# Optimization experiments

Hardware: AMD Instinct MI355X
Metric: run time of the kernel (lower is better)

The kernel has to match this reference:

```python
import jax, jax.numpy as jnp
import numpy as np

B, H, S, DK, DV = 2, 16, 2048, 128, 128


def setup_inputs() -> dict:
    key = jax.random.key(0)
    kq, kk, kv = jax.random.split(key, 3)
    query = jax.random.normal(kq, (B, H, S, DK), dtype=jnp.float32)
    k_ = jax.random.normal(kk, (B, H, S, DK), dtype=jnp.float32)
    value = jax.random.normal(kv, (B, H, S, DV), dtype=jnp.float32)
    # causal mask: True = masked out (upper triangle above diagonal)
    causal = ~jnp.tril(jnp.ones((S, S), dtype=bool))
    mask = jnp.broadcast_to(causal[None, None, :, :], (B, 1, S, S))
    return {"query": query, "key": k_, "value": value, "mask": mask}


def reference(query, key, value, mask):
    d_k = query.shape[-1]
    # scores: (B, H, Sq, Sk)
    scores = jnp.einsum("bhqd,bhkd->bhqk", query, key) / jnp.sqrt(jnp.float32(d_k))
    scores = jnp.where(mask, -jnp.inf, scores)
    attention_weights = jax.nn.softmax(scores, axis=-1)
    # dropout p=0.0 (eval) -> identity
    output = jnp.einsum("bhqk,bhkv->bhqv", attention_weights, value)
    return (output, attention_weights)
```

## Files before the change

kernel.cpp:

```cpp
#include <hip/hip_runtime.h>
#include <hip/hip_bf16.h>


typedef __attribute__((ext_vector_type(4))) float  f32x4;
typedef __attribute__((ext_vector_type(8))) short  short8;
typedef __attribute__((ext_vector_type(4))) short  short4v;

#define S_LEN 2048
#define DKK   128
#define QBLK  64
#define KBLK  64
#define NBH   32

__device__ __forceinline__ short f2bf(float f) {
    unsigned u = __builtin_bit_cast(unsigned, f);
    u += 0x7FFF + ((u >> 16) & 1);
    return (short)(u >> 16);
}

__device__ __forceinline__ void g2l16(const void* g, void* l) {
    __builtin_amdgcn_global_load_lds(
        (const __attribute__((address_space(1))) unsigned int*)g,
        (__attribute__((address_space(3))) unsigned int*)l, 16, 0, 0);
}


__global__ __launch_bounds__(256) void conv_k(const float* __restrict__ K,
                                              short* __restrict__ Kb) {
    const int NCH = NBH * S_LEN * (DKK / 8);
    for (int g = blockIdx.x * 256 + threadIdx.x; g < NCH; g += gridDim.x * 256) {
        const int row = g >> 4;
        const int c   = g & 15;
        const float* p = K + (size_t)row * DKK + c * 8;
        f32x4 a = *(const f32x4*)p;
        f32x4 b = *(const f32x4*)(p + 4);
        short8 r;
        #pragma unroll
        for (int j = 0; j < 4; ++j) {
            r[j]     = f2bf(a[j]);
            r[4 + j] = f2bf(b[j]);
        }
        *(short8*)(Kb + (size_t)row * DKK + (size_t)(c ^ (row & 7)) * 8) = r;
    }
}

__global__ __launch_bounds__(256) void conv_vt(const float* __restrict__ V,
                                               short* __restrict__ VT) {
    __shared__ short tile[64][130];
    const int bh = blockIdx.x >> 5;
    const int kt = blockIdx.x & 31;
    const float* Vb = V + ((size_t)bh * S_LEN + kt * 64) * DKK;
    const int t  = threadIdx.x;
    const int k8 = t >> 5, d0 = (t & 31) * 4;
    #pragma unroll
    for (int it = 0; it < 8; ++it) {
        int k = it * 8 + k8;
        f32x4 v = *(const f32x4*)(Vb + (size_t)k * DKK + d0);
        #pragma unroll
        for (int j = 0; j < 4; ++j) tile[k][d0 + j] = f2bf(v[j]);
    }
    __syncthreads();
    const int d = t >> 1, half = t & 1;
    short* outb = VT + (size_t)bh * DKK * S_LEN + (size_t)d * S_LEN + kt * 64;
    #pragma unroll
    for (int cc = 0; cc < 4; ++cc) {
        short8 r;
        #pragma unroll
        for (int j = 0; j < 8; ++j) r[j] = tile[half * 32 + cc * 8 + j][d];
        int cp = (half * 4 + cc) ^ (d & 7);
        *(short8*)(outb + cp * 8) = r;
    }
}


__global__ __launch_bounds__(256) void attn_main(
    const float* __restrict__ Qf, const short* __restrict__ Kb,
    const short* __restrict__ VT, float* __restrict__ O,
    float* __restrict__ W)
{
    __shared__ __align__(16) short kT[2][KBLK * DKK];
    __shared__ __align__(16) short vtT[2][DKK * KBLK];
    __shared__ __align__(16) short pT[4][16 * KBLK];

    const int tid  = threadIdx.x;
    const int lane = tid & 63;
    const int w    = tid >> 6;
    const int lg   = lane >> 4;
    const int lr   = lane & 15;
    const int s7   = lr & 7;

    const int bh = (blockIdx.x & 7) * 4 + ((blockIdx.x >> 3) & 3);
    const int qt = 31 - (blockIdx.x >> 5);
    const int q0 = qt * QBLK;
    const int qbase = q0 + w * 16;
    const int kend  = q0 + QBLK;
    const int ntk   = qt + 1;
    const int qg    = qbase + lr;

    const short* Kbh = Kb + (size_t)bh * S_LEN * DKK;
    const short* VTb = VT + (size_t)bh * DKK * S_LEN;
    float* Ob = O + (size_t)bh * S_LEN * DKK;
    float* Wb = W + (size_t)bh * S_LEN * S_LEN;

    const float QSCALE = 0.08838834764831845f * 1.4426950408889634f;
    short8 qf[4];
    {
        const float* qp = Qf + ((size_t)bh * S_LEN + qg) * DKK + lg * 8;
        #pragma unroll
        for (int ds = 0; ds < 4; ++ds) {
            f32x4 a = *(const f32x4*)(qp + ds * 32);
            f32x4 b = *(const f32x4*)(qp + ds * 32 + 4);
            short8 r;
            #pragma unroll
            for (int jj = 0; jj < 4; ++jj) {
                r[jj]     = f2bf(a[jj] * QSCALE);
                r[4 + jj] = f2bf(b[jj] * QSCALE);
            }
            qf[ds] = r;
        }
    }

    auto stage_k = [&](int buf, int kt_) {
        const char* gk = (const char*)(Kbh + (size_t)kt_ * KBLK * DKK);
        char* lk = (char*)kT[buf];
        #pragma unroll
        for (int i = 0; i < 4; ++i)
            g2l16(gk + i * 4096 + tid * 16, lk + i * 4096 + w * 1024);
    };
    auto stage_v = [&](int buf, int kt_) {
        const char* gv = (const char*)VTb + (size_t)kt_ * (KBLK * 2);
        char* lv = (char*)vtT[buf];
        #pragma unroll
        for (int i = 0; i < 4; ++i) {
            const int L = i * 4096 + tid * 16;
            g2l16(gv + (size_t)(L >> 7) * (S_LEN * 2) + (L & 127),
                  lv + i * 4096 + w * 1024);
        }
    };

    auto k_frag = [&](const char* kBc, int t, int ds) -> short8 {
        const int off = ((16 * t + lr) * 256 + ds * 64 + lg * 16) ^ (s7 << 4);
        return *(const short8*)(kBc + off);
    };

    float lsum = 0.f;
    int cur = 0;
    stage_k(0, 0);
    for (int kt_ = 0; kt_ < ntk; ++kt_) {
        __syncthreads();
        if (kt_ + 1 < ntk) stage_k(cur ^ 1, kt_ + 1);
        const int k0 = kt_ * KBLK;
        const char* kBc = (const char*)kT[cur];
        #pragma unroll
        for (int t = 0; t < 4; ++t) {
            f32x4 d = {0.f, 0.f, 0.f, 0.f};
            __builtin_amdgcn_s_setprio(1);
            #pragma unroll
            for (int ds = 0; ds < 4; ++ds)
                d = __builtin_amdgcn_mfma_f32_16x16x32_bf16(
                        k_frag(kBc, t, ds), qf[ds], d, 0, 0, 0);
            __builtin_amdgcn_s_setprio(0);
            const int kb = k0 + 16 * t + lg * 4;
            #pragma unroll
            for (int r = 0; r < 4; ++r)
                lsum += (kb + r <= qg) ? exp2f(d[r]) : 0.f;
        }
        cur ^= 1;
    }
    lsum += __shfl_xor(lsum, 16);
    lsum += __shfl_xor(lsum, 32);
    const float invl = 1.0f / lsum;

    f32x4 acc[8];
    #pragma unroll
    for (int ii = 0; ii < 8; ++ii) acc[ii] = (f32x4){0.f, 0.f, 0.f, 0.f};

    __syncthreads();
    cur = 0;
    stage_k(0, 0);
    stage_v(0, 0);
    for (int kt_ = 0; kt_ < ntk; ++kt_) {
        __syncthreads();
        if (kt_ + 1 < ntk) { stage_k(cur ^ 1, kt_ + 1); stage_v(cur ^ 1, kt_ + 1); }
        const int k0 = kt_ * KBLK;
        const char* kBc = (const char*)kT[cur];
        const char* vBc = (const char*)vtT[cur];
        char* pBc = (char*)pT[w];

        #pragma unroll
        for (int t = 0; t < 4; ++t) {
            f32x4 d = {0.f, 0.f, 0.f, 0.f};
            __builtin_amdgcn_s_setprio(1);
            #pragma unroll
            for (int ds = 0; ds < 4; ++ds)
                d = __builtin_amdgcn_mfma_f32_16x16x32_bf16(
                        k_frag(kBc, t, ds), qf[ds], d, 0, 0, 0);
            __builtin_amdgcn_s_setprio(0);
            const int kb = k0 + 16 * t + lg * 4;
            f32x4 pv;
            short4v pb;
            #pragma unroll
            for (int r = 0; r < 4; ++r) {
                const float p = (kb + r <= qg) ? exp2f(d[r]) * invl : 0.f;
                pv[r] = p;
                pb[r] = f2bf(p);
            }
            *(f32x4*)(Wb + (size_t)qg * S_LEN + kb) = pv;
            const int poff = lr * 128 + (((16 * t + lg * 4) * 2) ^ (s7 << 4));
            *(short4v*)(pBc + poff) = pb;
        }
        #pragma unroll
        for (int h = 0; h < 2; ++h) {
            const int poff = lr * 128 + ((h * 64 + lg * 16) ^ (s7 << 4));
            short8 pa = *(const short8*)(pBc + poff);
            __builtin_amdgcn_s_setprio(1);
            #pragma unroll
            for (int nt = 0; nt < 8; ++nt) {
                const int voff = (nt * 16 + lr) * 128 + ((h * 64 + lg * 16) ^ (s7 << 4));
                short8 vf = *(const short8*)(vBc + voff);
                acc[nt] = __builtin_amdgcn_mfma_f32_16x16x32_bf16(pa, vf, acc[nt], 0, 0, 0);
            }
            __builtin_amdgcn_s_setprio(0);
        }
        cur ^= 1;
    }

    #pragma unroll
    for (int nt = 0; nt < 8; ++nt)
        #pragma unroll
        for (int r = 0; r < 4; ++r)
            Ob[(size_t)(qbase + lg * 4 + r) * DKK + nt * 16 + lr] = acc[nt][r];

    const int zc = S_LEN - kend;
    if (zc > 0) {
        const int yo = tid >> 2;
        const int xo = tid & 3;
        float* wrow = Wb + (size_t)(q0 + yo) * S_LEN + kend;
        const f32x4 z = {0.f, 0.f, 0.f, 0.f};
        for (int c = xo * 4; c < zc; c += 16)
            *(f32x4*)(wrow + c) = z;
    }
}

extern "C" void kernel_launch(void* const* d_in, const int* in_sizes, int n_in,
                              void* d_out, int out_size, void* d_ws, size_t ws_size,
                              hipStream_t stream) {
    const float* Q = (const float*)d_in[0];
    const float* K = (const float*)d_in[1];
    const float* V = (const float*)d_in[2];
    float* O = (float*)d_out;
    float* W = (float*)d_out + (size_t)NBH * S_LEN * DKK;

    const size_t TEN = (size_t)NBH * S_LEN * DKK;
    short* Kb  = (short*)d_ws;
    short* VTw = Kb + TEN;

    conv_k <<<2048, 256, 0, stream>>>(K, Kb);
    conv_vt<<<1024, 256, 0, stream>>>(V, VTw);
    attn_main<<<1024, 256, 0, stream>>>(Q, Kb, VTw, O, W);
}
```

Before: 239.7 us.

## Double query tile per block to reuse staged K/V across two row groups

Each block now handles 128 query rows instead of 64, with every wave computing two 16-row groups so each K fragment loaded from LDS feeds two MFMAs and each V fragment is reused across both groups. This halves the number of blocks and the K/V global-to-LDS traffic per query row. The block-to-tile mapping is also changed to pair long and short causal tiles in launch order for load balance. In exchange, register pressure roughly doubles for accumulators and Q fragments, and there are fewer blocks to fill the device.

```diff
diff --git a/kernel.cpp b/kernel.cpp
--- a/kernel.cpp
+++ b/kernel.cpp
@@ -8,7 +8,7 @@
 
 #define S_LEN 2048
 #define DKK   128
-#define QBLK  64
+#define QBLK  128
 #define KBLK  64
 #define NBH   32
 
@@ -80,7 +80,7 @@
 {
     __shared__ __align__(16) short kT[2][KBLK * DKK];
     __shared__ __align__(16) short vtT[2][DKK * KBLK];
-    __shared__ __align__(16) short pT[4][16 * KBLK];
+    __shared__ __align__(16) short pT[4][32 * KBLK];
 
     const int tid  = threadIdx.x;
     const int lane = tid & 63;
@@ -89,13 +89,16 @@
     const int lr   = lane & 15;
     const int s7   = lr & 7;
 
-    const int bh = (blockIdx.x & 7) * 4 + ((blockIdx.x >> 3) & 3);
-    const int qt = 31 - (blockIdx.x >> 5);
-    const int q0 = qt * QBLK;
-    const int qbase = q0 + w * 16;
+    const int i     = blockIdx.x;
+    const int bh    = (i & 7) * 4 + ((i >> 3) & 3);
+    const int j     = (i >> 5) & 7;
+    const int qt    = (i >> 8) ? j : (15 - j);
+    const int q0    = qt * QBLK;
+    const int qbase = q0 + w * 32;
     const int kend  = q0 + QBLK;
-    const int ntk   = qt + 1;
-    const int qg    = qbase + lr;
+    const int ntk   = kend / KBLK;
+    const int qg0   = qbase + lr;
+    const int qg1   = qbase + 16 + lr;
 
     const short* Kbh = Kb + (size_t)bh * S_LEN * DKK;
     const short* VTb = VT + (size_t)bh * DKK * S_LEN;
@@ -103,9 +106,10 @@
     float* Wb = W + (size_t)bh * S_LEN * S_LEN;
 
     const float QSCALE = 0.08838834764831845f * 1.4426950408889634f;
-    short8 qf[4];
-    {
-        const float* qp = Qf + ((size_t)bh * S_LEN + qg) * DKK + lg * 8;
+    short8 qf[2][4];
+    #pragma unroll
+    for (int qh = 0; qh < 2; ++qh) {
+        const float* qp = Qf + ((size_t)bh * S_LEN + qbase + qh * 16 + lr) * DKK + lg * 8;
         #pragma unroll
         for (int ds = 0; ds < 4; ++ds) {
             f32x4 a = *(const f32x4*)(qp + ds * 32);
@@ -116,7 +120,7 @@
                 r[jj]     = f2bf(a[jj] * QSCALE);
                 r[4 + jj] = f2bf(b[jj] * QSCALE);
             }
-            qf[ds] = r;
+            qf[qh][ds] = r;
         }
     }
 
@@ -124,17 +128,17 @@
         const char* gk = (const char*)(Kbh + (size_t)kt_ * KBLK * DKK);
         char* lk = (char*)kT[buf];
         #pragma unroll
-        for (int i = 0; i < 4; ++i)
-            g2l16(gk + i * 4096 + tid * 16, lk + i * 4096 + w * 1024);
+        for (int ii = 0; ii < 4; ++ii)
+            g2l16(gk + ii * 4096 + tid * 16, lk + ii * 4096 + w * 1024);
     };
     auto stage_v = [&](int buf, int kt_) {
         const char* gv = (const char*)VTb + (size_t)kt_ * (KBLK * 2);
         char* lv = (char*)vtT[buf];
         #pragma unroll
-        for (int i = 0; i < 4; ++i) {
-            const int L = i * 4096 + tid * 16;
+        for (int ii = 0; ii < 4; ++ii) {
+            const int L = ii * 4096 + tid * 16;
             g2l16(gv + (size_t)(L >> 7) * (S_LEN * 2) + (L & 127),
-                  lv + i * 4096 + w * 1024);
+                  lv + ii * 4096 + w * 1024);
         }
     };
 
@@ -143,7 +147,7 @@
         return *(const short8*)(kBc + off);
     };
 
-    float lsum = 0.f;
+    float lsum[2] = {0.f, 0.f};
     int cur = 0;
     stage_k(0, 0);
     for (int kt_ = 0; kt_ < ntk; ++kt_) {
@@ -153,27 +157,37 @@
         const char* kBc = (const char*)kT[cur];
         #pragma unroll
         for (int t = 0; t < 4; ++t) {
-            f32x4 d = {0.f, 0.f, 0.f, 0.f};
+            f32x4 d0 = {0.f, 0.f, 0.f, 0.f};
+            f32x4 d1 = {0.f, 0.f, 0.f, 0.f};
             __builtin_amdgcn_s_setprio(1);
             #pragma unroll
-            for (int ds = 0; ds < 4; ++ds)
-                d = __builtin_amdgcn_mfma_f32_16x16x32_bf16(
-                        k_frag(kBc, t, ds), qf[ds], d, 0, 0, 0);
+            for (int ds = 0; ds < 4; ++ds) {
+                const short8 kf = k_frag(kBc, t, ds);
+                d0 = __builtin_amdgcn_mfma_f32_16x16x32_bf16(kf, qf[0][ds], d0, 0, 0, 0);
+                d1 = __builtin_amdgcn_mfma_f32_16x16x32_bf16(kf, qf[1][ds], d1, 0, 0, 0);
+            }
             __builtin_amdgcn_s_setprio(0);
             const int kb = k0 + 16 * t + lg * 4;
             #pragma unroll
-            for (int r = 0; r < 4; ++r)
-                lsum += (kb + r <= qg) ? exp2f(d[r]) : 0.f;
+            for (int r = 0; r < 4; ++r) {
+                lsum[0] += (kb + r <= qg0) ? exp2f(d0[r]) : 0.f;
+                lsum[1] += (kb + r <= qg1) ? exp2f(d1[r]) : 0.f;
+            }
         }
         cur ^= 1;
     }
-    lsum += __shfl_xor(lsum, 16);
-    lsum += __shfl_xor(lsum, 32);
-    const float invl = 1.0f / lsum;
-
-    f32x4 acc[8];
-    #pragma unroll
-    for (int ii = 0; ii < 8; ++ii) acc[ii] = (f32x4){0.f, 0.f, 0.f, 0.f};
+    lsum[0] += __shfl_xor(lsum[0], 16);
+    lsum[0] += __shfl_xor(lsum[0], 32);
+    lsum[1] += __shfl_xor(lsum[1], 16);
+    lsum[1] += __shfl_xor(lsum[1], 32);
+    const float invl0 = 1.0f / lsum[0];
+    const float invl1 = 1.0f / lsum[1];
+
+    f32x4 acc[2][8];
+    #pragma unroll
+    for (int qh = 0; qh < 2; ++qh)
+        #pragma unroll
+        for (int ii = 0; ii < 8; ++ii) acc[qh][ii] = (f32x4){0.f, 0.f, 0.f, 0.f};
 
     __syncthreads();
     cur = 0;
@@ -189,55 +203,73 @@
 
         #pragma unroll
         for (int t = 0; t < 4; ++t) {
-            f32x4 d = {0.f, 0.f, 0.f, 0.f};
+            f32x4 d0 = {0.f, 0.f, 0.f, 0.f};
+            f32x4 d1 = {0.f, 0.f, 0.f, 0.f};
             __builtin_amdgcn_s_setprio(1);
             #pragma unroll
-            for (int ds = 0; ds < 4; ++ds)
-                d = __builtin_amdgcn_mfma_f32_16x16x32_bf16(
-                        k_frag(kBc, t, ds), qf[ds], d, 0, 0, 0);
+            for (int ds = 0; ds < 4; ++ds) {
+                const short8 kf = k_frag(kBc, t, ds);
+                d0 = __builtin_amdgcn_mfma_f32_16x16x32_bf16(kf, qf[0][ds], d0, 0, 0, 0);
+                d1 = __builtin_amdgcn_mfma_f32_16x16x32_bf16(kf, qf[1][ds], d1, 0, 0, 0);
+            }
             __builtin_amdgcn_s_setprio(0);
             const int kb = k0 + 16 * t + lg * 4;
-            f32x4 pv;
-            short4v pb;
-            #pragma unroll
-            for (int r = 0; r < 4; ++r) {
-                const float p = (kb + r <= qg) ? exp2f(d[r]) * invl : 0.f;
-                pv[r] = p;
-                pb[r] = f2bf(p);
-            }
-            *(f32x4*)(Wb + (size_t)qg * S_LEN + kb) = pv;
-            const int poff = lr * 128 + (((16 * t + lg * 4) * 2) ^ (s7 << 4));
-            *(short4v*)(pBc + poff) = pb;
-        }
-        #pragma unroll
-        for (int h = 0; h < 2; ++h) {
-            const int poff = lr * 128 + ((h * 64 + lg * 16) ^ (s7 << 4));
-            short8 pa = *(const short8*)(pBc + poff);
-            __builtin_amdgcn_s_setprio(1);
-            #pragma unroll
-            for (int nt = 0; nt < 8; ++nt) {
-                const int voff = (nt * 16 + lr) * 128 + ((h * 64 + lg * 16) ^ (s7 << 4));
-                short8 vf = *(const short8*)(vBc + voff);
-                acc[nt] = __builtin_amdgcn_mfma_f32_16x16x32_bf16(pa, vf, acc[nt], 0, 0, 0);
-            }
-            __builtin_amdgcn_s_setprio(0);
+            const int kboff = ((16 * t + lg * 4) * 2) ^ (s7 << 4);
+            {
+                f32x4 pv; short4v pb;
+                #pragma unroll
+                for (int r = 0; r < 4; ++r) {
+                    const float p = (kb + r <= qg0) ? exp2f(d0[r]) * invl0 : 0.f;
+                    pv[r] = p; pb[r] = f2bf(p);
+                }
+                *(f32x4*)(Wb + (size_t)qg0 * S_LEN + kb) = pv;
+                *(short4v*)(pBc + lr * 128 + kboff) = pb;
+            }
+            {
+                f32x4 pv; short4v pb;
+                #pragma unroll
+                for (int r = 0; r < 4; ++r) {
+                    const float p = (kb + r <= qg1) ? exp2f(d1[r]) * invl1 : 0.f;
+                    pv[r] = p; pb[r] = f2bf(p);
+                }
+                *(f32x4*)(Wb + (size_t)qg1 * S_LEN + kb) = pv;
+                *(short4v*)(pBc + (16 + lr) * 128 + kboff) = pb;
+            }
+        }
+        #pragma unroll
+        for (int qh = 0; qh < 2; ++qh) {
+            #pragma unroll
+            for (int h = 0; h < 2; ++h) {
+                const int poff = (qh * 16 + lr) * 128 + ((h * 64 + lg * 16) ^ (s7 << 4));
+                short8 pa = *(const short8*)(pBc + poff);
+                __builtin_amdgcn_s_setprio(1);
+                #pragma unroll
+                for (int nt = 0; nt < 8; ++nt) {
+                    const int voff = (nt * 16 + lr) * 128 + ((h * 64 + lg * 16) ^ (s7 << 4));
+                    short8 vf = *(const short8*)(vBc + voff);
+                    acc[qh][nt] = __builtin_amdgcn_mfma_f32_16x16x32_bf16(pa, vf, acc[qh][nt], 0, 0, 0);
+                }
+                __builtin_amdgcn_s_setprio(0);
+            }
         }
         cur ^= 1;
     }
 
     #pragma unroll
-    for (int nt = 0; nt < 8; ++nt)
-        #pragma unroll
-        for (int r = 0; r < 4; ++r)
-            Ob[(size_t)(qbase + lg * 4 + r) * DKK + nt * 16 + lr] = acc[nt][r];
+    for (int qh = 0; qh < 2; ++qh)
+        #pragma unroll
+        for (int nt = 0; nt < 8; ++nt)
+            #pragma unroll
+            for (int r = 0; r < 4; ++r)
+                Ob[(size_t)(qbase + qh * 16 + lg * 4 + r) * DKK + nt * 16 + lr] = acc[qh][nt][r];
 
     const int zc = S_LEN - kend;
     if (zc > 0) {
-        const int yo = tid >> 2;
-        const int xo = tid & 3;
+        const int yo = tid >> 1;
+        const int xo = tid & 1;
         float* wrow = Wb + (size_t)(q0 + yo) * S_LEN + kend;
         const f32x4 z = {0.f, 0.f, 0.f, 0.f};
-        for (int c = xo * 4; c < zc; c += 16)
+        for (int c = xo * 4; c < zc; c += 8)
             *(f32x4*)(wrow + c) = z;
     }
 }
@@ -257,5 +289,5 @@
 
     conv_k <<<2048, 256, 0, stream>>>(K, Kb);
     conv_vt<<<1024, 256, 0, stream>>>(V, VTw);
-    attn_main<<<1024, 256, 0, stream>>>(Q, Kb, VTw, O, W);
-}
+    attn_main<<<NBH * (S_LEN / QBLK), 256, 0, stream>>>(Q, Kb, VTw, O, W);
+}
```

Result: no change. 243.6 us (+1.7%).
